# Optimization experiments

Hardware: AMD Instinct MI355X
Metric: run time of the kernel (lower is better)

## Reference

```python
import jax, jax.numpy as jnp
import numpy as np

B, T, N, C = 8, 16, 2048, 512


def setup_inputs() -> dict:
    key = jax.random.key(0)
    k1, k2, k3, k4, k5, k6 = jax.random.split(key, 6)
    return {
        "vd_s": jax.random.normal(k1, (B, T, C), dtype=jnp.float32),
        "vd_nodes": jax.random.normal(k2, (B, N, C), dtype=jnp.float32),
        # 1x1 conv weights initialized N(0, 0.01) as in the torch module
        "W1": jax.random.normal(k3, (C, C), dtype=jnp.float32) * 0.01,
        "b1": jax.random.normal(k4, (C,), dtype=jnp.float32) * 0.01,
        "W2": jax.random.normal(k5, (C, C), dtype=jnp.float32) * 0.01,
        "b2": jax.random.normal(k6, (C,), dtype=jnp.float32) * 0.01,
    }


def reference(vd_s, vd_nodes, W1, b1, W2, b2):
    # propagation_step = 1 (as in the original module)
    def per_graph(s, nodes):
        # s: [T, C] scene features, nodes: [N, C] node features
        out_scene = s.mean(axis=0)                     # [C]
        state = nodes                                  # [N, C]
        # 1x1 convs on [N, C, 1, 1] == per-node linear layers
        mat1 = state @ W1.T + b1                       # [N, C]
        mat2 = state @ W2.T + b2                       # [N, C]
        adj = mat1 @ mat2.T                            # [N, N]
        soft_adj = jax.nn.softmax(adj, axis=1)         # row-softmax (dim=1)
        new_state = soft_adj @ state + state           # message update + residual
        gp_out = new_state.mean(axis=0)                # [C]
        return jnp.concatenate([out_scene, gp_out], axis=0)  # [2C]

    return jax.vmap(per_graph)(vd_s, vd_nodes)         # [B, 2C]
```

## Files before the change

kernel.cpp:

```cpp
#include <hip/hip_runtime.h>

typedef __bf16 bf16;
typedef __bf16 bf16x8 __attribute__((ext_vector_type(8), aligned(16)));
typedef float  f32x4  __attribute__((ext_vector_type(4)));

#define B_ 8
#define T_ 16
#define N_ 2048
#define C_ 512

__device__ inline bf16x8 load8_f32(const float* p) {
    float4 a = *(const float4*)p;
    float4 b = *(const float4*)(p + 4);
    bf16x8 r;
    r[0] = (bf16)a.x; r[1] = (bf16)a.y; r[2] = (bf16)a.z; r[3] = (bf16)a.w;
    r[4] = (bf16)b.x; r[5] = (bf16)b.y; r[6] = (bf16)b.z; r[7] = (bf16)b.w;
    return r;
}

__device__ inline void gload_lds16(const bf16* g, bf16* l) {
    __builtin_amdgcn_global_load_lds(
        (const __attribute__((address_space(1))) void*)g,
        (__attribute__((address_space(3))) void*)l, 16, 0, 0);
}

__global__ __launch_bounds__(256) void k_prep(
    const float* __restrict__ vd_s, const float* __restrict__ nodes,
    const float* __restrict__ W1, const float* __restrict__ W2,
    float* __restrict__ out, bf16* __restrict__ nodes_bf,
    bf16* __restrict__ W1t, bf16* __restrict__ W2t) {
    __shared__ float sh[32 * 33];
    const int bx = blockIdx.x, tid = threadIdx.x;
    if (bx < 2048) {
        size_t i = ((size_t)bx * 256 + tid) * 16;
        *(bf16x8*)(nodes_bf + i)     = load8_f32(nodes + i);
        *(bf16x8*)(nodes_bf + i + 8) = load8_f32(nodes + i + 8);
    } else if (bx < 2064) {
        int gt = (bx - 2048) * 256 + tid;
        int b = gt >> 9, c = gt & 511;
        float s = 0.f;
#pragma unroll
        for (int t = 0; t < T_; ++t) s += vd_s[(size_t)b * T_ * C_ + t * C_ + c];
        out[b * 2 * C_ + c] = s * (1.0f / T_);
    } else {
        const float* W = (bx < 2320) ? W1 : W2;
        bf16* Wt = (bx < 2320) ? W1t : W2t;
        int idx = (bx < 2320) ? bx - 2064 : bx - 2320;
        int bxx = (idx & 15) * 32, byy = (idx >> 4) * 32;
        int tx = tid & 31, ty = tid >> 5;
#pragma unroll
        for (int r = 0; r < 32; r += 8)
            sh[(ty + r) * 33 + tx] = W[(size_t)(byy + ty + r) * C_ + bxx + tx];
        __syncthreads();
#pragma unroll
        for (int r = 0; r < 32; r += 8)
            Wt[(size_t)(bxx + ty + r) * C_ + byy + tx] = (bf16)sh[tx * 33 + ty + r];
    }
}

__global__ void k_q(const float* __restrict__ b1, const bf16* __restrict__ W2t,
                    float* __restrict__ q) {
    int wid = threadIdx.x >> 6, lane = threadIdx.x & 63;
    int c = blockIdx.x * 4 + wid;
    bf16x8 v8 = *(const bf16x8*)(W2t + (size_t)c * C_ + lane * 8);
    float s = 0.f;
#pragma unroll
    for (int i = 0; i < 8; ++i) s += (float)v8[i] * b1[lane * 8 + i];
#pragma unroll
    for (int m = 32; m; m >>= 1) s += __shfl_xor(s, m);
    if (lane == 0) q[c] = s;
}

template <bool EXPOUT>
__global__ __launch_bounds__(256) void gemm_nt(
    const bf16* __restrict__ A, size_t strideA,
    const bf16* __restrict__ Bm, size_t strideB,
    const float* __restrict__ bias,
    bf16* __restrict__ C, size_t strideC,
    int N, int K) {
    __shared__ __attribute__((aligned(16))) bf16 lA[128 * 64];
    __shared__ __attribute__((aligned(16))) bf16 lB[128 * 64];
    const int tid = threadIdx.x;
    const int lane = tid & 63, w = tid >> 6;
    const int wm = w >> 1, wn = w & 1;
    const int z = blockIdx.z;
    const int bm = blockIdx.x * 128, bn = blockIdx.y * 128;
    const bf16* Ab = A + (size_t)z * strideA;
    const bf16* Bb = Bm + (size_t)z * strideB;

    f32x4 acc[4][4];
#pragma unroll
    for (int i = 0; i < 4; ++i)
#pragma unroll
        for (int j = 0; j < 4; ++j) acc[i][j] = f32x4{0.f, 0.f, 0.f, 0.f};

    const int nkt = K >> 6;
    for (int kt = 0; kt < nkt; ++kt) {
#pragma unroll
        for (int c = 0; c < 4; ++c) {
            int ca = c * 256 + tid;
            int row = ca >> 3;
            int qd = (ca & 7) ^ (row & 7);
            gload_lds16(Ab + (size_t)(bm + row) * K + kt * 64 + qd * 8,
                        lA + c * 2048 + w * 512);
            gload_lds16(Bb + (size_t)(bn + row) * K + kt * 64 + qd * 8,
                        lB + c * 2048 + w * 512);
        }
        __syncthreads();

        bf16x8 af[2][4], bfr[2][4];
#pragma unroll
        for (int ks = 0; ks < 2; ++ks) {
            int y = ks * 4 + (lane >> 4);
#pragma unroll
            for (int i = 0; i < 4; ++i) {
                int ra = wm * 64 + i * 16 + (lane & 15);
                int rb = wn * 64 + i * 16 + (lane & 15);
                af[ks][i]  = *(const bf16x8*)&lA[ra * 64 + ((y ^ (ra & 7)) * 8)];
                bfr[ks][i] = *(const bf16x8*)&lB[rb * 64 + ((y ^ (rb & 7)) * 8)];
            }
        }
#pragma unroll
        for (int ks = 0; ks < 2; ++ks)
#pragma unroll
            for (int i = 0; i < 4; ++i)
#pragma unroll
                for (int j = 0; j < 4; ++j)
                    acc[i][j] = __builtin_amdgcn_mfma_f32_16x16x32_bf16(
                        af[ks][i], bfr[ks][j], acc[i][j], 0, 0, 0);
        __syncthreads();
    }

    bf16* Cb = C + (size_t)z * strideC;
#pragma unroll
    for (int i = 0; i < 4; ++i) {
#pragma unroll
        for (int j = 0; j < 4; ++j) {
            int col = bn + wn * 64 + j * 16 + (lane & 15);
            float bv = (!EXPOUT && bias) ? bias[col] : 0.f;
#pragma unroll
            for (int r = 0; r < 4; ++r) {
                int row = bm + wm * 64 + i * 16 + (lane >> 4) * 4 + r;
                float v = acc[i][j][r];
                if (EXPOUT) v = __expf(fminf(v, 30.f));
                else        v = v + bv;
                Cb[(size_t)row * N + col] = (bf16)v;
            }
        }
    }
}

__global__ __launch_bounds__(256) void k_w2(const bf16* __restrict__ P,
                                            float* __restrict__ wpart) {
    __shared__ float rp[16 * 256];
    __shared__ float ri[16];
    const int tid = threadIdx.x;
    const int s = blockIdx.x, b = blockIdx.y;
    const bf16* Pb = P + (size_t)b * N_ * N_ + (size_t)s * 16 * N_;
    const int j0 = tid * 8;
    bf16x8 v[16];
#pragma unroll
    for (int r = 0; r < 16; ++r) {
        v[r] = *(const bf16x8*)&Pb[(size_t)r * N_ + j0];
        float t = 0.f;
#pragma unroll
        for (int e = 0; e < 8; ++e) t += (float)v[r][e];
        rp[r * 256 + tid] = t;
    }
    __syncthreads();
    {
        int row = tid >> 4, seg = tid & 15;
        float t = 0.f;
#pragma unroll
        for (int k = 0; k < 16; ++k) t += rp[row * 256 + seg + 16 * k];
#pragma unroll
        for (int m = 8; m; m >>= 1) t += __shfl_xor(t, m);
        if (seg == 0) ri[row] = 1.0f / t;
    }
    __syncthreads();
    float acc8[8] = {0.f, 0.f, 0.f, 0.f, 0.f, 0.f, 0.f, 0.f};
#pragma unroll
    for (int r = 0; r < 16; ++r) {
        float rr = ri[r];
#pragma unroll
        for (int e = 0; e < 8; ++e) acc8[e] += rr * (float)v[r][e];
    }
    float* wp = wpart + ((size_t)b * 128 + s) * (size_t)N_;
#pragma unroll
    for (int e = 0; e < 8; ++e) wp[j0 + e] = acc8[e];
}

__global__ __launch_bounds__(256) void k_gp(const bf16* __restrict__ nodes_bf,
                                            const float* __restrict__ wpart,
                                            float* __restrict__ gppart) {
    __shared__ float wred[4][64];
    __shared__ float wsh[64];
    __shared__ float gred[4][512];
    const int tid = threadIdx.x;
    const int slab = blockIdx.x, b = blockIdx.y;
    const int jj = tid & 63, sg = tid >> 6;
    float wacc = 0.f;
    for (int s = sg; s < 128; s += 4)
        wacc += wpart[((size_t)b * 128 + s) * N_ + slab * 64 + jj];
    wred[sg][jj] = wacc;
    __syncthreads();
    if (tid < 64)
        wsh[tid] = wred[0][tid] + wred[1][tid] + wred[2][tid] + wred[3][tid] + 1.0f;
    __syncthreads();
    const int j0 = slab * 64;
    const int cc = (tid & 63) * 8, jr = tid >> 6;
    const bf16* nb = nodes_bf + (size_t)b * N_ * C_;
    float acc8[8] = {0.f, 0.f, 0.f, 0.f, 0.f, 0.f, 0.f, 0.f};
    for (int j = jr; j < 64; j += 4) {
        float wj = wsh[j];
        bf16x8 nv = *(const bf16x8*)&nb[(size_t)(j0 + j) * C_ + cc];
#pragma unroll
        for (int e = 0; e < 8; ++e) acc8[e] += wj * (float)nv[e];
    }
#pragma unroll
    for (int e = 0; e < 8; ++e) gred[jr][cc + e] = acc8[e];
    __syncthreads();
    if (tid < 64) {
#pragma unroll
        for (int e = 0; e < 8; ++e) {
            int c = tid * 8 + e;
            gppart[((size_t)slab * 8 + b) * C_ + c] =
                gred[0][c] + gred[1][c] + gred[2][c] + gred[3][c];
        }
    }
}

__global__ void k_fin(const float* __restrict__ gppart, float* __restrict__ out) {
    int gt = blockIdx.x * 256 + threadIdx.x;
    int b = gt >> 9, c = gt & 511;
    float s = 0.f;
#pragma unroll
    for (int k = 0; k < 32; ++k) s += gppart[((size_t)k * 8 + b) * C_ + c];
    out[b * 2 * C_ + C_ + c] = s * (1.0f / N_);
}

extern "C" void kernel_launch(void* const* d_in, const int* in_sizes, int n_in,
                              void* d_out, int out_size, void* d_ws, size_t ws_size,
                              hipStream_t stream) {
    const float* vd_s  = (const float*)d_in[0];
    const float* nodes = (const float*)d_in[1];
    const float* W1    = (const float*)d_in[2];
    const float* b1    = (const float*)d_in[3];
    const float* W2    = (const float*)d_in[4];
    float* out = (float*)d_out;

    char* ws = (char*)d_ws;
    bf16*  nodes_bf = (bf16*)(ws);
    bf16*  H2       = (bf16*)(ws + ((size_t)16 << 20));
    float* wpart    = (float*)(ws + ((size_t)16 << 20));
    bf16*  P        = (bf16*)(ws + ((size_t)32 << 20));
    bf16*  W1t      = (bf16*)(ws + ((size_t)96 << 20));
    bf16*  W2t      = (bf16*)(ws + ((size_t)96 << 20) + (512u << 10));
    bf16*  Gt       = (bf16*)(ws + ((size_t)96 << 20) + (1024u << 10));
    char*  fbase    = ws + ((size_t)96 << 20) + (1536u << 10);
    float* q        = (float*)(fbase);
    float* gppart   = (float*)(fbase + 4096);

    k_prep<<<2576, 256, 0, stream>>>(vd_s, nodes, W1, W2,
                                     out, nodes_bf, W1t, W2t);
    k_q<<<128, 256, 0, stream>>>(b1, W2t, q);

    gemm_nt<false><<<dim3(4, 4, 1), 256, 0, stream>>>(
        W2t, 0, W1t, 0, nullptr, Gt, 0, C_, C_);
    gemm_nt<false><<<dim3(16, 4, 8), 256, 0, stream>>>(
        nodes_bf, (size_t)N_ * C_, Gt, 0, q,
        H2, (size_t)N_ * C_, C_, C_);
    gemm_nt<true><<<dim3(16, 16, 8), 256, 0, stream>>>(
        H2, (size_t)N_ * C_, nodes_bf, (size_t)N_ * C_, nullptr,
        P, (size_t)N_ * N_, N_, C_);

    k_w2<<<dim3(128, 8), 256, 0, stream>>>(P, wpart);
    k_gp<<<dim3(32, 8), 256, 0, stream>>>(nodes_bf, wpart, gppart);
    k_fin<<<16, 256, 0, stream>>>(gppart, out);
}
```

Before: 126.0 us.

## Replace attention-logit GEMM with 256x256 tiled, phased, double-buffered MFMA kernel

Adds a dedicated kernel for the batched exp(H2·nodesᵀ) GEMM. It uses 256x256 output tiles with 8 waves and double-buffered LDS filled via direct global-to-LDS loads with XOR swizzling. The K loop is split into four MFMA phases that interleave half-tile prefetches, with barriers and s_setprio, and block IDs are remapped for locality. The goal is more data reuse per tile and hiding load latency behind MFMA work in the dominant N×N GEMM. The cost is heavy register pressure from 32 accumulators per lane and rigid manual vmcnt accounting, which could break if the load counts shift.

Result: faster. 115.4 us (-8.4%).

```diff
diff --git a/kernel.cpp b/kernel.cpp
--- a/kernel.cpp
+++ b/kernel.cpp
@@ -71,7 +71,6 @@
     if (lane == 0) q[c] = s;
 }
 
-template <bool EXPOUT>
 __global__ __launch_bounds__(256) void gemm_nt(
     const bf16* __restrict__ A, size_t strideA,
     const bf16* __restrict__ Bm, size_t strideB,
@@ -137,17 +136,179 @@
 #pragma unroll
         for (int j = 0; j < 4; ++j) {
             int col = bn + wn * 64 + j * 16 + (lane & 15);
-            float bv = (!EXPOUT && bias) ? bias[col] : 0.f;
+            float bv = bias ? bias[col] : 0.f;
 #pragma unroll
             for (int r = 0; r < 4; ++r) {
                 int row = bm + wm * 64 + i * 16 + (lane >> 4) * 4 + r;
-                float v = acc[i][j][r];
-                if (EXPOUT) v = __expf(fminf(v, 30.f));
-                else        v = v + bv;
-                Cb[(size_t)row * N + col] = (bf16)v;
-            }
-        }
-    }
+                Cb[(size_t)row * N + col] = (bf16)(acc[i][j][r] + bv);
+            }
+        }
+    }
+}
+
+__global__ __launch_bounds__(512, 2) void gemm256p(
+    const bf16* __restrict__ A, const bf16* __restrict__ Bm,
+    bf16* __restrict__ P) {
+    __shared__ __attribute__((aligned(16))) bf16 ls[2][2][16384];
+    const int tid = threadIdx.x;
+    const int lane = tid & 63, w = tid >> 6;
+    const int wm = w >> 2, wn = w & 3;
+    const int id = blockIdx.x;
+    const int sw = (id & 7) * 64 + (id >> 3);
+    const int z = sw >> 6, tt = sw & 63;
+    const int bm = (tt >> 3) * 256, bn = (tt & 7) * 256;
+    const bf16* Ab = A + (size_t)z * N_ * C_;
+    const bf16* Bb = Bm + (size_t)z * N_ * C_;
+
+    f32x4 acc[8][4];
+#pragma unroll
+    for (int i = 0; i < 8; ++i)
+#pragma unroll
+        for (int j = 0; j < 4; ++j) acc[i][j] = f32x4{0.f, 0.f, 0.f, 0.f};
+
+#define STAGE_H(MATP, BASE, h, kt_, buf_, abi)                                    \
+    {                                                                             \
+        _Pragma("unroll")                                                         \
+        for (int sl = 0; sl < 2; ++sl) {                                          \
+            int cc = sl * 512 + tid;                                              \
+            int row = (h) * 128 + (cc >> 3);                                      \
+            int qd = (cc & 7) ^ (row & 7);                                        \
+            gload_lds16(MATP + (size_t)((BASE) + row) * C_ + (kt_) * 64 + qd * 8, \
+                        &ls[buf_][abi][((h) * 1024 + sl * 512 + w * 64) * 8]);    \
+        }                                                                         \
+    }
+#define PH_SYNC_MFMA                                                    \
+    __builtin_amdgcn_s_barrier();                                       \
+    asm volatile("s_waitcnt lgkmcnt(0)" ::: "memory");                  \
+    __builtin_amdgcn_sched_barrier(0);                                  \
+    __builtin_amdgcn_s_setprio(1);
+
+    STAGE_H(Ab, bm, 0, 0, 0, 0); STAGE_H(Ab, bm, 1, 0, 0, 0);
+    STAGE_H(Bb, bn, 0, 0, 0, 1); STAGE_H(Bb, bn, 1, 0, 0, 1);
+    STAGE_H(Bb, bn, 0, 1, 1, 1); STAGE_H(Bb, bn, 1, 1, 1, 1);
+    asm volatile("s_waitcnt vmcnt(4)" ::: "memory");
+    __builtin_amdgcn_s_barrier();
+
+#pragma unroll
+    for (int j = 0; j < 8; ++j) {
+        const int cur = j & 1, nxt = cur ^ 1;
+        const bf16* lA = &ls[cur][0][0];
+        const bf16* lB = &ls[cur][1][0];
+        bf16x8 af[4][2], b0[2][2], b1v[2][2];
+
+#pragma unroll
+        for (int i = 0; i < 4; ++i) {
+            int ra = wm * 128 + i * 16 + (lane & 15);
+#pragma unroll
+            for (int ks = 0; ks < 2; ++ks) {
+                int y = ks * 4 + (lane >> 4);
+                af[i][ks] = *(const bf16x8*)&lA[ra * 64 + ((y ^ (ra & 7)) * 8)];
+            }
+        }
+#pragma unroll
+        for (int jj = 0; jj < 2; ++jj) {
+            int rb = wn * 64 + jj * 16 + (lane & 15);
+#pragma unroll
+            for (int ks = 0; ks < 2; ++ks) {
+                int y = ks * 4 + (lane >> 4);
+                b0[jj][ks] = *(const bf16x8*)&lB[rb * 64 + ((y ^ (rb & 7)) * 8)];
+            }
+        }
+        if (j < 7) STAGE_H(Ab, bm, 0, j + 1, nxt, 0);
+        PH_SYNC_MFMA
+#pragma unroll
+        for (int ks = 0; ks < 2; ++ks)
+#pragma unroll
+            for (int i = 0; i < 4; ++i)
+#pragma unroll
+                for (int jj = 0; jj < 2; ++jj)
+                    acc[i][jj] = __builtin_amdgcn_mfma_f32_16x16x32_bf16(
+                        af[i][ks], b0[jj][ks], acc[i][jj], 0, 0, 0);
+        __builtin_amdgcn_s_setprio(0);
+        __builtin_amdgcn_s_barrier();
+
+#pragma unroll
+        for (int jj = 0; jj < 2; ++jj) {
+            int rb = wn * 64 + 32 + jj * 16 + (lane & 15);
+#pragma unroll
+            for (int ks = 0; ks < 2; ++ks) {
+                int y = ks * 4 + (lane >> 4);
+                b1v[jj][ks] = *(const bf16x8*)&lB[rb * 64 + ((y ^ (rb & 7)) * 8)];
+            }
+        }
+        if (j < 7) STAGE_H(Ab, bm, 1, j + 1, nxt, 0);
+        PH_SYNC_MFMA
+#pragma unroll
+        for (int ks = 0; ks < 2; ++ks)
+#pragma unroll
+            for (int i = 0; i < 4; ++i)
+#pragma unroll
+                for (int jj = 0; jj < 2; ++jj)
+                    acc[i][2 + jj] = __builtin_amdgcn_mfma_f32_16x16x32_bf16(
+                        af[i][ks], b1v[jj][ks], acc[i][2 + jj], 0, 0, 0);
+        __builtin_amdgcn_s_setprio(0);
+        __builtin_amdgcn_s_barrier();
+
+#pragma unroll
+        for (int i = 0; i < 4; ++i) {
+            int ra = wm * 128 + 64 + i * 16 + (lane & 15);
+#pragma unroll
+            for (int ks = 0; ks < 2; ++ks) {
+                int y = ks * 4 + (lane >> 4);
+                af[i][ks] = *(const bf16x8*)&lA[ra * 64 + ((y ^ (ra & 7)) * 8)];
+            }
+        }
+        if (j < 6) STAGE_H(Bb, bn, 0, j + 2, cur, 1);
+        PH_SYNC_MFMA
+#pragma unroll
+        for (int ks = 0; ks < 2; ++ks)
+#pragma unroll
+            for (int i = 0; i < 4; ++i)
+#pragma unroll
+                for (int jj = 0; jj < 2; ++jj)
+                    acc[4 + i][jj] = __builtin_amdgcn_mfma_f32_16x16x32_bf16(
+                        af[i][ks], b0[jj][ks], acc[4 + i][jj], 0, 0, 0);
+        __builtin_amdgcn_s_setprio(0);
+        __builtin_amdgcn_s_barrier();
+
+        if (j < 6) {
+            STAGE_H(Bb, bn, 1, j + 2, cur, 1);
+            asm volatile("s_waitcnt vmcnt(4)" ::: "memory");
+        } else if (j == 6) {
+            asm volatile("s_waitcnt vmcnt(0)" ::: "memory");
+        }
+        __builtin_amdgcn_s_barrier();
+        __builtin_amdgcn_s_setprio(1);
+#pragma unroll
+        for (int ks = 0; ks < 2; ++ks)
+#pragma unroll
+            for (int i = 0; i < 4; ++i)
+#pragma unroll
+                for (int jj = 0; jj < 2; ++jj)
+                    acc[4 + i][2 + jj] = __builtin_amdgcn_mfma_f32_16x16x32_bf16(
+                        af[i][ks], b1v[jj][ks], acc[4 + i][2 + jj], 0, 0, 0);
+        __builtin_amdgcn_s_setprio(0);
+        __builtin_amdgcn_s_barrier();
+    }
+
+    bf16* Pb = P + (size_t)z * N_ * N_;
+#pragma unroll
+    for (int fi = 0; fi < 8; ++fi) {
+#pragma unroll
+        for (int fj = 0; fj < 4; ++fj) {
+            int roff = (fi >> 2) * 64 + (fi & 3) * 16;
+            int coff = (fj >> 1) * 32 + (fj & 1) * 16;
+            int col = bn + wn * 64 + coff + (lane & 15);
+#pragma unroll
+            for (int r = 0; r < 4; ++r) {
+                int row = bm + wm * 128 + roff + (lane >> 4) * 4 + r;
+                float v = __expf(fminf(acc[fi][fj][r], 30.f));
+                Pb[(size_t)row * N_ + col] = (bf16)v;
+            }
+        }
+    }
+#undef STAGE_H
+#undef PH_SYNC_MFMA
 }
 
 __global__ __launch_bounds__(256) void k_w2(const bf16* __restrict__ P,
@@ -265,14 +426,12 @@
                                      out, nodes_bf, W1t, W2t);
     k_q<<<128, 256, 0, stream>>>(b1, W2t, q);
 
-    gemm_nt<false><<<dim3(4, 4, 1), 256, 0, stream>>>(
+    gemm_nt<<<dim3(4, 4, 1), 256, 0, stream>>>(
         W2t, 0, W1t, 0, nullptr, Gt, 0, C_, C_);
-    gemm_nt<false><<<dim3(16, 4, 8), 256, 0, stream>>>(
+    gemm_nt<<<dim3(16, 4, 8), 256, 0, stream>>>(
         nodes_bf, (size_t)N_ * C_, Gt, 0, q,
         H2, (size_t)N_ * C_, C_, C_);
-    gemm_nt<true><<<dim3(16, 16, 8), 256, 0, stream>>>(
-        H2, (size_t)N_ * C_, nodes_bf, (size_t)N_ * C_, nullptr,
-        P, (size_t)N_ * N_, N_, C_);
+    gemm256p<<<512, 512, 0, stream>>>(H2, nodes_bf, P);
 
     k_w2<<<dim3(128, 8), 256, 0, stream>>>(P, wpart);
     k_gp<<<dim3(32, 8), 256, 0, stream>>>(nodes_bf, wpart, gppart);
```
